# Performance work log

Hardware: AMD Instinct MI355X
Metric: run time of the kernel (lower is better)

The kernel has to match this reference:

```python
import jax, jax.numpy as jnp
import numpy as np

TAU = 1.0  # forward() default temperature

def setup_inputs() -> dict:
    key = jax.random.key(0)
    ks = jax.random.split(key, 6)
    B, T, I, H, O = 1024, 512, 100, 150, 3
    s_ih = 1.0 / np.sqrt(H)  # torch nn.RNN init scale (uniform +-1/sqrt(H)); randn used for simplicity of magnitude
    return {
        "x": jax.random.normal(ks[0], (B, T, I), dtype=jnp.float32),
        "h0": jax.random.normal(ks[1], (B, H), dtype=jnp.float32),  # init=True: h ~ N(0,1)
        "g": jax.random.normal(ks[2], (B, T, O), dtype=jnp.float32),  # gumbel noise (externalized)
        "W_ih": jax.random.normal(ks[3], (H, I), dtype=jnp.float32) * s_ih,
        "W_hh": jax.random.normal(ks[4], (H, H), dtype=jnp.float32) * s_ih,
        "W_fc": jax.random.normal(ks[5], (O, H), dtype=jnp.float32) * s_ih,
    }

def _rnn_relu(x, h0, W_ih, W_hh):
    # x: [B,T,I]; precompute input projection once (batched GEMM), then scan over time.
    xw = jnp.einsum("bti,hi->tbh", x, W_ih)  # [T,B,H]
    def step(h, xw_t):
        h = jax.nn.relu(xw_t + h @ W_hh.T)
        return h, h
    _, hs = jax.lax.scan(step, h0, xw)  # hs: [T,B,H]
    return jnp.transpose(hs, (1, 0, 2))  # [B,T,H]

def reference(x, h0, g, W_ih, W_hh, W_fc):
    hidden = _rnn_relu(x, h0, W_ih, W_hh)           # [B,T,H]
    logits = jnp.einsum("bth,oh->bto", hidden, W_fc)  # [B,T,O]
    # F.gumbel_softmax(hard=True): softmax((logits+g)/tau), straight-through one-hot
    y_soft = jax.nn.softmax((logits + g) / TAU, axis=-1)
    idx = jnp.argmax(y_soft, axis=-1)
    y_hard = jax.nn.one_hot(idx, logits.shape[-1], dtype=y_soft.dtype)
    out = y_soft + jax.lax.stop_gradient(y_hard - y_soft)
    return (out, hidden, logits)
```

## Files before the change

kernel.cpp:

```cpp
#include <hip/hip_runtime.h>

constexpr int NB = 1024;
constexpr int NT = 512;
constexpr int NI = 100;
constexpr int NH = 150;
constexpr int NO = 3;
constexpr int KP = 256;
constexpr int XOFF = 152;
constexpr int ROWS = 2;
constexpr int KG   = 16;
constexpr int NCH  = 4;
constexpr int NJ   = 5;
constexpr int NTH  = 512;

template<int CTRL>
__device__ __forceinline__ float dpp_add(float v) {
    int t = __builtin_amdgcn_update_dpp(0, __float_as_int(v), CTRL, 0xF, 0xF, true);
    return v + __int_as_float(t);
}

__global__ __launch_bounds__(NTH, 2)
void rnn_fused(const float* __restrict__ x, const float* __restrict__ h0,
               const float* __restrict__ g, const float* __restrict__ Wih,
               const float* __restrict__ Whh, const float* __restrict__ Wfc,
               float* __restrict__ out, float* __restrict__ hidden,
               float* __restrict__ logits)
{
    __shared__ __align__(16) float hx[2][ROWS * KP];
    __shared__ float lg[2][ROWS][4];

    const int tid  = threadIdx.x;
    const int lane = tid & 63;
    const int wv   = tid >> 6;
    const int kg   = lane & 15;
    const int oq   = lane >> 4;
    const int oi   = wv * 4 + oq;
    const int row0 = blockIdx.x * ROWS;

    float Wreg[NJ][NCH][4];
#pragma unroll
    for (int j = 0; j < NJ; ++j) {
        const int o = oi + 32 * j;
#pragma unroll
        for (int i = 0; i < NCH; ++i) {
#pragma unroll
            for (int q = 0; q < 4; ++q) {
                const int k = 4 * (kg + KG * i) + q;
                float v = 0.f;
                if (o < NH) {
                    if (k < NH) v = Whh[o * NH + k];
                    else if (k >= XOFF && k < XOFF + NI) v = Wih[o * NI + (k - XOFF)];
                } else if (o < NH + NO) {
                    if (k < NH) v = Wfc[(o - NH) * NH + k];
                }
                Wreg[j][i][q] = v;
            }
        }
    }

    for (int e = tid; e < ROWS * NH; e += NTH) {
        int b = e / NH, k = e - b * NH;
        hx[0][b * KP + k] = h0[(row0 + b) * NH + k];
    }
    for (int e = tid; e < ROWS * NI; e += NTH) {
        int b = e / NI, i = e - b * NI;
        hx[0][b * KP + XOFF + i] = x[((size_t)(row0 + b) * NT + 0) * NI + i];
    }
    if (tid < 2 * ROWS * 6) {
        int u = tid; int f = u / (ROWS * 6); u -= f * (ROWS * 6);
        int b = u / 6, z = u - b * 6;
        int k = (z < 2) ? (NH + z) : (252 + z - 2);
        hx[f][b * KP + k] = 0.f;
    }
    __syncthreads();

    const int xb = (tid / 25) & 1, xq = tid - (tid / 25) * 25;
    const float* xrow = x + ((size_t)(row0 + xb) * NT) * NI + 4 * xq;
    float* hidb = hidden + ((size_t)(row0 + (kg & 1)) * NT) * NH;
    const float* grow = g + ((size_t)(row0 + (tid & 1)) * NT) * NO;
    const size_t emitb = ((size_t)(row0 + (tid & 1)) * NT) * NO;

    auto stepf = [&](int t, const float* __restrict__ cur, float* __restrict__ nxt,
                     float (*__restrict__ lgb)[4]) {
        float4 xp = make_float4(0.f, 0.f, 0.f, 0.f);
        const bool do_x = (tid < 50) && (t < NT - 1);
        if (do_x) xp = *reinterpret_cast<const float4*>(xrow + (size_t)(t + 1) * NI);
        float g0 = 0.f, g1 = 0.f, g2 = 0.f;
        const bool do_e = (tid < ROWS) && (t >= 1);
        if (do_e) {
            const float* gp = grow + (size_t)(t - 1) * NO;
            g0 = gp[0]; g1 = gp[1]; g2 = gp[2];
        }

        const float4* cur4 = reinterpret_cast<const float4*>(cur) + kg;
        float acc[NJ][ROWS];
#pragma unroll
        for (int j = 0; j < NJ; ++j)
#pragma unroll
            for (int b = 0; b < ROWS; ++b) acc[j][b] = 0.f;

#pragma unroll
        for (int i = 0; i < NCH; ++i) {
#pragma unroll
            for (int b = 0; b < ROWS; ++b) {
                const float4 hv = cur4[b * (KP / 4) + KG * i];
#pragma unroll
                for (int j = 0; j < NJ; ++j) {
                    acc[j][b] += Wreg[j][i][0] * hv.x;
                    acc[j][b] += Wreg[j][i][1] * hv.y;
                    acc[j][b] += Wreg[j][i][2] * hv.z;
                    acc[j][b] += Wreg[j][i][3] * hv.w;
                }
            }
        }

#pragma unroll
        for (int j = 0; j < NJ; ++j)
#pragma unroll
            for (int b = 0; b < ROWS; ++b) {
                float v = acc[j][b];
                v = dpp_add<0xB1>(v);
                v = dpp_add<0x4E>(v);
                v = dpp_add<0x141>(v);
                v = dpp_add<0x140>(v);
                acc[j][b] = v;
            }

        if (kg < ROWS) {
            const int b = kg;
#pragma unroll
            for (int j = 0; j < NJ; ++j) {
                const int o = oi + 32 * j;
                if (o < NH) {
                    if (t < NT) {
                        float v = fmaxf(acc[j][b], 0.f);
                        nxt[b * KP + o] = v;
                        hidb[(size_t)t * NH + o] = v;
                    }
                } else if (o < NH + NO) {
                    lgb[b][o - NH] = acc[j][b];
                }
            }
        }
        if (do_x) *reinterpret_cast<float4*>(nxt + xb * KP + XOFF + 4 * xq) = xp;
        __syncthreads();

        if (do_e) {
            float l0 = lgb[tid][0], l1 = lgb[tid][1], l2 = lgb[tid][2];
            float s0 = l0 + g0, s1 = l1 + g1, s2 = l2 + g2;
            int am = 0; float best = s0;
            if (s1 > best) { best = s1; am = 1; }
            if (s2 > best) { am = 2; }
            size_t base = emitb + (size_t)(t - 1) * NO;
            out[base + 0] = (am == 0) ? 1.f : 0.f;
            out[base + 1] = (am == 1) ? 1.f : 0.f;
            out[base + 2] = (am == 2) ? 1.f : 0.f;
            logits[base + 0] = l0;
            logits[base + 1] = l1;
            logits[base + 2] = l2;
        }
    };

    for (int t = 0; t < NT; t += 2) {
        stepf(t,     hx[0], hx[1], lg[0]);
        stepf(t + 1, hx[1], hx[0], lg[1]);
    }
    stepf(NT, hx[0], hx[1], lg[0]);
}

extern "C" void kernel_launch(void* const* d_in, const int* in_sizes, int n_in,
                              void* d_out, int out_size, void* d_ws, size_t ws_size,
                              hipStream_t stream) {
    const float* x   = (const float*)d_in[0];
    const float* h0  = (const float*)d_in[1];
    const float* g   = (const float*)d_in[2];
    const float* Wih = (const float*)d_in[3];
    const float* Whh = (const float*)d_in[4];
    const float* Wfc = (const float*)d_in[5];

    float* out    = (float*)d_out;
    float* hidden = out + (size_t)NB * NT * NO;
    float* logits = hidden + (size_t)NB * NT * NH;

    hipLaunchKernelGGL(rnn_fused, dim3(NB / ROWS), dim3(NTH), 0, stream,
                       x, h0, g, Wih, Whh, Wfc, out, hidden, logits);
}
```

Before: 1.829 ms.

## Split input projection into separate GEMM kernel and shrink recurrent matvec

Adds a GEMM kernel that computes x·W_ih^T for all timesteps up front into a workspace buffer. The recurrent kernel then handles only the 150-wide hidden state, with 4 batch rows per block and 8-lane reductions instead of 16. The old fused kernel stays as a fallback when no workspace is available. This shortens the serial critical path per step, at the cost of roughly 300MB of extra global traffic to write and read the projection buffer.

```diff
diff --git a/kernel.cpp b/kernel.cpp
--- a/kernel.cpp
+++ b/kernel.cpp
@@ -5,13 +5,6 @@
 constexpr int NI = 100;
 constexpr int NH = 150;
 constexpr int NO = 3;
-constexpr int KP = 256;
-constexpr int XOFF = 152;
-constexpr int ROWS = 2;
-constexpr int KG   = 16;
-constexpr int NCH  = 4;
-constexpr int NJ   = 5;
-constexpr int NTH  = 512;
 
 template<int CTRL>
 __device__ __forceinline__ float dpp_add(float v) {
@@ -19,6 +12,204 @@
     return v + __int_as_float(t);
 }
 
+constexpr int GB = 128, GH = 32, GT = 256;
+__global__ __launch_bounds__(GT, 2)
+void xw_gemm(const float* __restrict__ x, const float* __restrict__ Wih,
+             float* __restrict__ xw)
+{
+    __shared__ __align__(16) float xt[GB * NI];
+    __shared__ __align__(16) float ot[GB * GH];
+    const int tid = threadIdx.x;
+    const int b0 = blockIdx.x * GB, t = blockIdx.y, h0 = blockIdx.z * GH;
+
+    for (int e = tid; e < GB * (NI / 4); e += GT) {
+        int r = e / 25, c = e - r * 25;
+        reinterpret_cast<float4*>(xt)[r * 25 + c] =
+            reinterpret_cast<const float4*>(x + ((size_t)(b0 + r) * NT + t) * NI)[c];
+    }
+    __syncthreads();
+
+    const int row = tid & (GB - 1);
+    const int hbase = __builtin_amdgcn_readfirstlane(h0 + (tid >> 7) * 16);
+    const float* wrow[16];
+#pragma unroll
+    for (int j = 0; j < 16; ++j) {
+        int h = hbase + j;
+        wrow[j] = Wih + (size_t)(h < NH ? h : NH - 1) * NI;
+    }
+    float acc[16];
+#pragma unroll
+    for (int j = 0; j < 16; ++j) acc[j] = 0.f;
+
+    const float4* xr = reinterpret_cast<const float4*>(xt) + row * 25;
+#pragma unroll 5
+    for (int k4 = 0; k4 < 25; ++k4) {
+        const float4 xv = xr[k4];
+#pragma unroll
+        for (int j = 0; j < 16; ++j) {
+            const float4 wv = reinterpret_cast<const float4*>(wrow[j])[k4];
+            acc[j] += wv.x * xv.x;
+            acc[j] += wv.y * xv.y;
+            acc[j] += wv.z * xv.z;
+            acc[j] += wv.w * xv.w;
+        }
+    }
+    const int hg = (tid >> 7) * 16;
+#pragma unroll
+    for (int j = 0; j < 16; ++j) ot[row * GH + hg + j] = acc[j];
+    __syncthreads();
+
+    for (int e = tid; e < GB * 16; e += GT) {
+        int r = e >> 4, p = e & 15, h = h0 + 2 * p;
+        if (h < NH) {
+            float2 v = *reinterpret_cast<const float2*>(&ot[r * GH + 2 * p]);
+            *reinterpret_cast<float2*>(&xw[((size_t)t * NB + b0 + r) * NH + h]) = v;
+        }
+    }
+}
+
+constexpr int KP2 = 160, ROWS2 = 4, NTH2 = 512;
+__global__ __launch_bounds__(NTH2, 2)
+void rnn_rec(const float* __restrict__ xw, const float* __restrict__ h0v,
+             const float* __restrict__ g, const float* __restrict__ Whh,
+             const float* __restrict__ Wfc, float* __restrict__ out,
+             float* __restrict__ hidden, float* __restrict__ logits)
+{
+    __shared__ __align__(16) float hx[2][ROWS2 * KP2];
+    __shared__ float lg[2][ROWS2][4];
+
+    const int tid = threadIdx.x, lane = tid & 63, wv = tid >> 6;
+    const int kg = lane & 7, oq = lane >> 3, oi = wv * 8 + oq;
+    const int row0 = blockIdx.x * ROWS2;
+
+    float Wreg[3][5][4];
+#pragma unroll
+    for (int j = 0; j < 3; ++j) {
+        const int o = oi + 64 * j;
+#pragma unroll
+        for (int i = 0; i < 5; ++i)
+#pragma unroll
+            for (int q = 0; q < 4; ++q) {
+                const int k = 4 * (kg + 8 * i) + q;
+                float v = 0.f;
+                if (k < NH) {
+                    if (o < NH) v = Whh[o * NH + k];
+                    else if (o < NH + NO) v = Wfc[(o - NH) * NH + k];
+                }
+                Wreg[j][i][q] = v;
+            }
+    }
+
+    for (int e = tid; e < ROWS2 * NH; e += NTH2) {
+        int b = e / NH, k = e - b * NH;
+        hx[0][b * KP2 + k] = h0v[(row0 + b) * NH + k];
+    }
+    if (tid < 2 * ROWS2 * 10) {
+        int u = tid, f = u / (ROWS2 * 10); u -= f * (ROWS2 * 10);
+        int b = u / 10, z = u - b * 10;
+        hx[f][b * KP2 + NH + z] = 0.f;
+    }
+    __syncthreads();
+
+    const float* xwb = xw + (size_t)(row0 + (kg & 3)) * NH;
+    float* hidb = hidden + (size_t)(row0 + (kg & 3)) * NT * NH;
+    const float* grow = g + (size_t)(row0 + (tid & 3)) * NT * NO;
+    const size_t emitb = (size_t)(row0 + (tid & 3)) * NT * NO;
+
+    auto stepf = [&](int t, const float* __restrict__ cur, float* __restrict__ nxt,
+                     float (*__restrict__ lgb)[4]) {
+        float xwv[3] = {0.f, 0.f, 0.f};
+        const bool wr = (kg < ROWS2);
+        if (wr && t < NT) {
+            const float* xp = xwb + (size_t)t * (NB * NH);
+#pragma unroll
+            for (int j = 0; j < 3; ++j) {
+                const int o = oi + 64 * j;
+                if (o < NH) xwv[j] = xp[o];
+            }
+        }
+        float g0 = 0.f, g1 = 0.f, g2 = 0.f;
+        const bool de = (tid < ROWS2) && (t >= 1);
+        if (de) {
+            const float* gp = grow + (size_t)(t - 1) * NO;
+            g0 = gp[0]; g1 = gp[1]; g2 = gp[2];
+        }
+
+        const float4* cur4 = reinterpret_cast<const float4*>(cur) + kg;
+        float acc[3][ROWS2];
+#pragma unroll
+        for (int j = 0; j < 3; ++j)
+#pragma unroll
+            for (int b = 0; b < ROWS2; ++b) acc[j][b] = 0.f;
+
+#pragma unroll
+        for (int i = 0; i < 5; ++i)
+#pragma unroll
+            for (int b = 0; b < ROWS2; ++b) {
+                const float4 hv = cur4[b * (KP2 / 4) + 8 * i];
+#pragma unroll
+                for (int j = 0; j < 3; ++j) {
+                    acc[j][b] += Wreg[j][i][0] * hv.x;
+                    acc[j][b] += Wreg[j][i][1] * hv.y;
+                    acc[j][b] += Wreg[j][i][2] * hv.z;
+                    acc[j][b] += Wreg[j][i][3] * hv.w;
+                }
+            }
+
+#pragma unroll
+        for (int j = 0; j < 3; ++j)
+#pragma unroll
+            for (int b = 0; b < ROWS2; ++b) {
+                float v = acc[j][b];
+                v = dpp_add<0xB1>(v);
+                v = dpp_add<0x4E>(v);
+                v = dpp_add<0x141>(v);
+                acc[j][b] = v;
+            }
+
+        if (wr) {
+            const int b = kg;
+#pragma unroll
+            for (int j = 0; j < 3; ++j) {
+                const int o = oi + 64 * j;
+                if (o < NH) {
+                    if (t < NT) {
+                        float v = fmaxf(acc[j][b] + xwv[j], 0.f);
+                        nxt[b * KP2 + o] = v;
+                        hidb[(size_t)t * NH + o] = v;
+                    }
+                } else if (o < NH + NO) {
+                    lgb[b][o - NH] = acc[j][b];
+                }
+            }
+        }
+        __syncthreads();
+
+        if (de) {
+            float l0 = lgb[tid][0], l1 = lgb[tid][1], l2 = lgb[tid][2];
+            float s0 = l0 + g0, s1 = l1 + g1, s2 = l2 + g2;
+            int am = 0; float best = s0;
+            if (s1 > best) { best = s1; am = 1; }
+            if (s2 > best) { am = 2; }
+            size_t base = emitb + (size_t)(t - 1) * NO;
+            out[base + 0] = (am == 0) ? 1.f : 0.f;
+            out[base + 1] = (am == 1) ? 1.f : 0.f;
+            out[base + 2] = (am == 2) ? 1.f : 0.f;
+            logits[base + 0] = l0;
+            logits[base + 1] = l1;
+            logits[base + 2] = l2;
+        }
+    };
+
+    for (int t = 0; t < NT; t += 2) {
+        stepf(t,     hx[0], hx[1], lg[0]);
+        stepf(t + 1, hx[1], hx[0], lg[1]);
+    }
+    stepf(NT, hx[0], hx[1], lg[0]);
+}
+
+namespace fb {
+constexpr int KP = 256, XOFF = 152, ROWS = 2, KG = 16, NCH = 4, NJ = 5, NTH = 512;
 __global__ __launch_bounds__(NTH, 2)
 void rnn_fused(const float* __restrict__ x, const float* __restrict__ h0,
                const float* __restrict__ g, const float* __restrict__ Wih,
@@ -28,21 +219,15 @@
 {
     __shared__ __align__(16) float hx[2][ROWS * KP];
     __shared__ float lg[2][ROWS][4];
-
-    const int tid  = threadIdx.x;
-    const int lane = tid & 63;
-    const int wv   = tid >> 6;
-    const int kg   = lane & 15;
-    const int oq   = lane >> 4;
-    const int oi   = wv * 4 + oq;
+    const int tid = threadIdx.x, lane = tid & 63, wv = tid >> 6;
+    const int kg = lane & 15, oq = lane >> 4, oi = wv * 4 + oq;
     const int row0 = blockIdx.x * ROWS;
-
     float Wreg[NJ][NCH][4];
 #pragma unroll
     for (int j = 0; j < NJ; ++j) {
         const int o = oi + 32 * j;
 #pragma unroll
-        for (int i = 0; i < NCH; ++i) {
+        for (int i = 0; i < NCH; ++i)
 #pragma unroll
             for (int q = 0; q < 4; ++q) {
                 const int k = 4 * (kg + KG * i) + q;
@@ -55,9 +240,7 @@
                 }
                 Wreg[j][i][q] = v;
             }
-        }
-    }
-
+    }
     for (int e = tid; e < ROWS * NH; e += NTH) {
         int b = e / NH, k = e - b * NH;
         hx[0][b * KP + k] = h0[(row0 + b) * NH + k];
@@ -73,13 +256,11 @@
         hx[f][b * KP + k] = 0.f;
     }
     __syncthreads();
-
     const int xb = (tid / 25) & 1, xq = tid - (tid / 25) * 25;
     const float* xrow = x + ((size_t)(row0 + xb) * NT) * NI + 4 * xq;
     float* hidb = hidden + ((size_t)(row0 + (kg & 1)) * NT) * NH;
     const float* grow = g + ((size_t)(row0 + (tid & 1)) * NT) * NO;
     const size_t emitb = ((size_t)(row0 + (tid & 1)) * NT) * NO;
-
     auto stepf = [&](int t, const float* __restrict__ cur, float* __restrict__ nxt,
                      float (*__restrict__ lgb)[4]) {
         float4 xp = make_float4(0.f, 0.f, 0.f, 0.f);
@@ -91,16 +272,14 @@
             const float* gp = grow + (size_t)(t - 1) * NO;
             g0 = gp[0]; g1 = gp[1]; g2 = gp[2];
         }
-
         const float4* cur4 = reinterpret_cast<const float4*>(cur) + kg;
         float acc[NJ][ROWS];
 #pragma unroll
         for (int j = 0; j < NJ; ++j)
 #pragma unroll
             for (int b = 0; b < ROWS; ++b) acc[j][b] = 0.f;
-
-#pragma unroll
-        for (int i = 0; i < NCH; ++i) {
+#pragma unroll
+        for (int i = 0; i < NCH; ++i)
 #pragma unroll
             for (int b = 0; b < ROWS; ++b) {
                 const float4 hv = cur4[b * (KP / 4) + KG * i];
@@ -112,8 +291,6 @@
                     acc[j][b] += Wreg[j][i][3] * hv.w;
                 }
             }
-        }
-
 #pragma unroll
         for (int j = 0; j < NJ; ++j)
 #pragma unroll
@@ -125,7 +302,6 @@
                 v = dpp_add<0x140>(v);
                 acc[j][b] = v;
             }
-
         if (kg < ROWS) {
             const int b = kg;
 #pragma unroll
@@ -144,7 +320,6 @@
         }
         if (do_x) *reinterpret_cast<float4*>(nxt + xb * KP + XOFF + 4 * xq) = xp;
         __syncthreads();
-
         if (do_e) {
             float l0 = lgb[tid][0], l1 = lgb[tid][1], l2 = lgb[tid][2];
             float s0 = l0 + g0, s1 = l1 + g1, s2 = l2 + g2;
@@ -160,12 +335,12 @@
             logits[base + 2] = l2;
         }
     };
-
     for (int t = 0; t < NT; t += 2) {
         stepf(t,     hx[0], hx[1], lg[0]);
         stepf(t + 1, hx[1], hx[0], lg[1]);
     }
     stepf(NT, hx[0], hx[1], lg[0]);
+}
 }
 
 extern "C" void kernel_launch(void* const* d_in, const int* in_sizes, int n_in,
@@ -182,6 +357,15 @@
     float* hidden = out + (size_t)NB * NT * NO;
     float* logits = hidden + (size_t)NB * NT * NH;
 
-    hipLaunchKernelGGL(rnn_fused, dim3(NB / ROWS), dim3(NTH), 0, stream,
-                       x, h0, g, Wih, Whh, Wfc, out, hidden, logits);
-}
+    const size_t need = (size_t)NT * NB * NH * sizeof(float);
+    if (d_ws != nullptr && ws_size >= need) {
+        float* xwbuf = (float*)d_ws;
+        hipLaunchKernelGGL(xw_gemm, dim3(NB / GB, NT, (NH + GH - 1) / GH), dim3(GT),
+                           0, stream, x, Wih, xwbuf);
+        hipLaunchKernelGGL(rnn_rec, dim3(NB / ROWS2), dim3(NTH2), 0, stream,
+                           xwbuf, h0, g, Whh, Wfc, out, hidden, logits);
+    } else {
+        hipLaunchKernelGGL(fb::rnn_fused, dim3(NB / fb::ROWS), dim3(fb::NTH), 0, stream,
+                           x, h0, g, Wih, Whh, Wfc, out, hidden, logits);
+    }
+}
```

Measured after the change: 2.213 ms. +21.0%, slower.

## Split input projection into separate GEMM kernel and prefetch xw asynchronously

Applied to the files above, without the earlier changes.

Moves the x·W_ih projection out of the sequential recurrence into a parallel GEMM kernel that writes a [T,B,H] buffer in the workspace. The recurrent kernel then handles one batch row per 256-thread block, multiplies only W_hh (K=150 instead of 250), and prefetches the next timestep's projected input into LDS with global_load_lds. This shortens the serial critical path per step and raises block count. The cost is an extra ~300MB workspace round trip to global memory. The old fused kernel stays as a fallback when the workspace is too small.

```diff
diff --git a/kernel.cpp b/kernel.cpp
--- a/kernel.cpp
+++ b/kernel.cpp
@@ -5,13 +5,6 @@
 constexpr int NI = 100;
 constexpr int NH = 150;
 constexpr int NO = 3;
-constexpr int KP = 256;
-constexpr int XOFF = 152;
-constexpr int ROWS = 2;
-constexpr int KG   = 16;
-constexpr int NCH  = 4;
-constexpr int NJ   = 5;
-constexpr int NTH  = 512;
 
 template<int CTRL>
 __device__ __forceinline__ float dpp_add(float v) {
@@ -19,6 +12,182 @@
     return v + __int_as_float(t);
 }
 
+__device__ __forceinline__ void async_copy_f32(const float* src, float* lds_dst) {
+    __builtin_amdgcn_global_load_lds(
+        (const __attribute__((address_space(1))) void*)src,
+        (__attribute__((address_space(3))) void*)lds_dst, 4, 0, 0);
+}
+
+constexpr int XR = 64, XTH = 512;
+__global__ __launch_bounds__(XTH, 1)
+void xw_gemm(const float* __restrict__ x, const float* __restrict__ Wih,
+             float* __restrict__ xw)
+{
+    __shared__ __align__(16) float Wl[152 * NI];
+    __shared__ float xT[XR * 101];
+    __shared__ float ot[XR * 151];
+    const int tid = threadIdx.x;
+    const int b0 = blockIdx.x * XR;
+    const int t  = blockIdx.y;
+
+    for (int e = tid; e < 152 * 25; e += XTH) {
+        int wr = e / 25, k4 = e - wr * 25;
+        float4 v = make_float4(0.f, 0.f, 0.f, 0.f);
+        if (wr < NH) v = *reinterpret_cast<const float4*>(Wih + (size_t)wr * NI + 4 * k4);
+        *reinterpret_cast<float4*>(&Wl[wr * NI + 4 * k4]) = v;
+    }
+    for (int e = tid; e < XR * 25; e += XTH) {
+        int r = e / 25, k4 = e - r * 25;
+        float4 v = *reinterpret_cast<const float4*>(x + ((size_t)(b0 + r) * NT + t) * NI + 4 * k4);
+        xT[r * 101 + 4 * k4 + 0] = v.x; xT[r * 101 + 4 * k4 + 1] = v.y;
+        xT[r * 101 + 4 * k4 + 2] = v.z; xT[r * 101 + 4 * k4 + 3] = v.w;
+    }
+    __syncthreads();
+
+    const int row = tid & 63;
+    const int wv  = tid >> 6;
+    float acc[19];
+#pragma unroll
+    for (int j = 0; j < 19; ++j) acc[j] = 0.f;
+    const float* xr = &xT[row * 101];
+    const float* wb = &Wl[19 * wv * NI];
+    for (int k4 = 0; k4 < 25; ++k4) {
+        const float x0 = xr[4 * k4 + 0], x1 = xr[4 * k4 + 1];
+        const float x2 = xr[4 * k4 + 2], x3 = xr[4 * k4 + 3];
+#pragma unroll
+        for (int j = 0; j < 19; ++j) {
+            const float4 w4 = *reinterpret_cast<const float4*>(&wb[j * NI + 4 * k4]);
+            acc[j] += w4.x * x0; acc[j] += w4.y * x1;
+            acc[j] += w4.z * x2; acc[j] += w4.w * x3;
+        }
+    }
+#pragma unroll
+    for (int j = 0; j < 19; ++j) {
+        const int h = 19 * wv + j;
+        if (h < NH) ot[row * 151 + h] = acc[j];
+    }
+    __syncthreads();
+
+    for (int e = tid; e < XR * 75; e += XTH) {
+        int r = e / 75, c2 = e - r * 75;
+        float2 v = make_float2(ot[r * 151 + 2 * c2], ot[r * 151 + 2 * c2 + 1]);
+        *reinterpret_cast<float2*>(&xw[((size_t)t * NB + b0 + r) * NH + 2 * c2]) = v;
+    }
+}
+
+constexpr int RTH = 256;
+__global__ __launch_bounds__(RTH, 4)
+void rnn_rec(const float* __restrict__ xw, const float* __restrict__ h0v,
+             const float* __restrict__ g, const float* __restrict__ Whh,
+             const float* __restrict__ Wfc, float* __restrict__ out,
+             float* __restrict__ hidden, float* __restrict__ logits)
+{
+    __shared__ __align__(16) float hx[2][160];
+    __shared__ __align__(16) float xq[2][152];
+    __shared__ float lg[2][4];
+
+    const int tid = threadIdx.x, lane = tid & 63, wv = tid >> 6;
+    const int kg = lane & 7, oq = lane >> 3;
+    const int oi = wv * 8 + oq;
+    const int row = blockIdx.x;
+
+    float Wreg[5][5][4];
+#pragma unroll
+    for (int j = 0; j < 5; ++j) {
+        const int o = oi + 32 * j;
+#pragma unroll
+        for (int i = 0; i < 5; ++i)
+#pragma unroll
+            for (int q = 0; q < 4; ++q) {
+                const int k = 4 * (kg + 8 * i) + q;
+                float v = 0.f;
+                if (k < NH) {
+                    if (o < NH) v = Whh[o * NH + k];
+                    else if (o < NH + NO) v = Wfc[(o - NH) * NH + k];
+                }
+                Wreg[j][i][q] = v;
+            }
+    }
+
+    if (tid < NH) hx[0][tid] = h0v[(size_t)row * NH + tid];
+    if (tid < 20) { int f = tid / 10, z = tid - 10 * (tid / 10); hx[f][NH + z] = 0.f; }
+    {
+        const float* s = xw + (size_t)row * NH;
+        if (tid < 64) { async_copy_f32(s + tid, &xq[0][0]); async_copy_f32(s + 64 + tid, &xq[0][64]); }
+        if (tid < 22) async_copy_f32(s + 128 + tid, &xq[0][128]);
+    }
+    __syncthreads();
+
+    float* hidb = hidden + (size_t)row * NT * NH;
+    const float* gb = g + (size_t)row * NT * NO;
+    float* ob = out + (size_t)row * NT * NO;
+    float* lb = logits + (size_t)row * NT * NO;
+
+    auto stepf = [&](int t, const float* __restrict__ cur, float* __restrict__ nxt,
+                     float* __restrict__ lgc, const float* __restrict__ xv,
+                     float* __restrict__ xnxt) {
+        if (t + 1 < NT) {
+            const float* s = xw + ((size_t)(t + 1) * NB + row) * NH;
+            if (tid < 64) { async_copy_f32(s + tid, xnxt); async_copy_f32(s + 64 + tid, xnxt + 64); }
+            if (tid < 22) async_copy_f32(s + 128 + tid, xnxt + 128);
+        }
+        float acc[5];
+#pragma unroll
+        for (int j = 0; j < 5; ++j) acc[j] = 0.f;
+        const float4* c4 = reinterpret_cast<const float4*>(cur);
+#pragma unroll
+        for (int i = 0; i < 5; ++i) {
+            const float4 hv = c4[kg + 8 * i];
+#pragma unroll
+            for (int j = 0; j < 5; ++j) {
+                acc[j] += Wreg[j][i][0] * hv.x; acc[j] += Wreg[j][i][1] * hv.y;
+                acc[j] += Wreg[j][i][2] * hv.z; acc[j] += Wreg[j][i][3] * hv.w;
+            }
+        }
+#pragma unroll
+        for (int j = 0; j < 5; ++j) {
+            float v = acc[j];
+            v = dpp_add<0xB1>(v); v = dpp_add<0x4E>(v); v = dpp_add<0x141>(v);
+            acc[j] = v;
+        }
+        if (kg == 0) {
+#pragma unroll
+            for (int j = 0; j < 5; ++j) {
+                const int o = oi + 32 * j;
+                if (o < NH) {
+                    if (t < NT) {
+                        float v = fmaxf(acc[j] + xv[o], 0.f);
+                        nxt[o] = v;
+                        hidb[(size_t)t * NH + o] = v;
+                    }
+                } else if (o < NH + NO) lgc[o - NH] = acc[j];
+            }
+        }
+        __syncthreads();
+        if (tid == 0 && t >= 1) {
+            float l0 = lgc[0], l1 = lgc[1], l2 = lgc[2];
+            const float* gp = gb + (size_t)(t - 1) * NO;
+            float s0 = l0 + gp[0], s1 = l1 + gp[1], s2 = l2 + gp[2];
+            int am = 0; float best = s0;
+            if (s1 > best) { best = s1; am = 1; }
+            if (s2 > best) am = 2;
+            size_t base = (size_t)(t - 1) * NO;
+            ob[base + 0] = (am == 0) ? 1.f : 0.f;
+            ob[base + 1] = (am == 1) ? 1.f : 0.f;
+            ob[base + 2] = (am == 2) ? 1.f : 0.f;
+            lb[base + 0] = l0; lb[base + 1] = l1; lb[base + 2] = l2;
+        }
+    };
+
+    for (int t = 0; t < NT; t += 2) {
+        stepf(t,     hx[0], hx[1], lg[0], xq[0], xq[1]);
+        stepf(t + 1, hx[1], hx[0], lg[1], xq[1], xq[0]);
+    }
+    stepf(NT, hx[0], hx[1], lg[0], xq[0], xq[1]);
+}
+
+namespace fb {
+constexpr int KP = 256, XOFF = 152, ROWS = 2, KG = 16, NCH = 4, NJ = 5, NTH = 512;
 __global__ __launch_bounds__(NTH, 2)
 void rnn_fused(const float* __restrict__ x, const float* __restrict__ h0,
                const float* __restrict__ g, const float* __restrict__ Wih,
@@ -28,21 +197,15 @@
 {
     __shared__ __align__(16) float hx[2][ROWS * KP];
     __shared__ float lg[2][ROWS][4];
-
-    const int tid  = threadIdx.x;
-    const int lane = tid & 63;
-    const int wv   = tid >> 6;
-    const int kg   = lane & 15;
-    const int oq   = lane >> 4;
-    const int oi   = wv * 4 + oq;
+    const int tid = threadIdx.x, lane = tid & 63, wv = tid >> 6;
+    const int kg = lane & 15, oq = lane >> 4, oi = wv * 4 + oq;
     const int row0 = blockIdx.x * ROWS;
-
     float Wreg[NJ][NCH][4];
 #pragma unroll
     for (int j = 0; j < NJ; ++j) {
         const int o = oi + 32 * j;
 #pragma unroll
-        for (int i = 0; i < NCH; ++i) {
+        for (int i = 0; i < NCH; ++i)
 #pragma unroll
             for (int q = 0; q < 4; ++q) {
                 const int k = 4 * (kg + KG * i) + q;
@@ -55,9 +218,7 @@
                 }
                 Wreg[j][i][q] = v;
             }
-        }
-    }
-
+    }
     for (int e = tid; e < ROWS * NH; e += NTH) {
         int b = e / NH, k = e - b * NH;
         hx[0][b * KP + k] = h0[(row0 + b) * NH + k];
@@ -73,13 +234,11 @@
         hx[f][b * KP + k] = 0.f;
     }
     __syncthreads();
-
     const int xb = (tid / 25) & 1, xq = tid - (tid / 25) * 25;
     const float* xrow = x + ((size_t)(row0 + xb) * NT) * NI + 4 * xq;
     float* hidb = hidden + ((size_t)(row0 + (kg & 1)) * NT) * NH;
     const float* grow = g + ((size_t)(row0 + (tid & 1)) * NT) * NO;
     const size_t emitb = ((size_t)(row0 + (tid & 1)) * NT) * NO;
-
     auto stepf = [&](int t, const float* __restrict__ cur, float* __restrict__ nxt,
                      float (*__restrict__ lgb)[4]) {
         float4 xp = make_float4(0.f, 0.f, 0.f, 0.f);
@@ -91,16 +250,14 @@
             const float* gp = grow + (size_t)(t - 1) * NO;
             g0 = gp[0]; g1 = gp[1]; g2 = gp[2];
         }
-
         const float4* cur4 = reinterpret_cast<const float4*>(cur) + kg;
         float acc[NJ][ROWS];
 #pragma unroll
         for (int j = 0; j < NJ; ++j)
 #pragma unroll
             for (int b = 0; b < ROWS; ++b) acc[j][b] = 0.f;
-
-#pragma unroll
-        for (int i = 0; i < NCH; ++i) {
+#pragma unroll
+        for (int i = 0; i < NCH; ++i)
 #pragma unroll
             for (int b = 0; b < ROWS; ++b) {
                 const float4 hv = cur4[b * (KP / 4) + KG * i];
@@ -112,20 +269,15 @@
                     acc[j][b] += Wreg[j][i][3] * hv.w;
                 }
             }
-        }
-
 #pragma unroll
         for (int j = 0; j < NJ; ++j)
 #pragma unroll
             for (int b = 0; b < ROWS; ++b) {
                 float v = acc[j][b];
-                v = dpp_add<0xB1>(v);
-                v = dpp_add<0x4E>(v);
-                v = dpp_add<0x141>(v);
-                v = dpp_add<0x140>(v);
+                v = dpp_add<0xB1>(v); v = dpp_add<0x4E>(v);
+                v = dpp_add<0x141>(v); v = dpp_add<0x140>(v);
                 acc[j][b] = v;
             }
-
         if (kg < ROWS) {
             const int b = kg;
 #pragma unroll
@@ -144,7 +296,6 @@
         }
         if (do_x) *reinterpret_cast<float4*>(nxt + xb * KP + XOFF + 4 * xq) = xp;
         __syncthreads();
-
         if (do_e) {
             float l0 = lgb[tid][0], l1 = lgb[tid][1], l2 = lgb[tid][2];
             float s0 = l0 + g0, s1 = l1 + g1, s2 = l2 + g2;
@@ -160,12 +311,12 @@
             logits[base + 2] = l2;
         }
     };
-
     for (int t = 0; t < NT; t += 2) {
         stepf(t,     hx[0], hx[1], lg[0]);
         stepf(t + 1, hx[1], hx[0], lg[1]);
     }
     stepf(NT, hx[0], hx[1], lg[0]);
+}
 }
 
 extern "C" void kernel_launch(void* const* d_in, const int* in_sizes, int n_in,
@@ -182,6 +333,15 @@
     float* hidden = out + (size_t)NB * NT * NO;
     float* logits = hidden + (size_t)NB * NT * NH;
 
-    hipLaunchKernelGGL(rnn_fused, dim3(NB / ROWS), dim3(NTH), 0, stream,
-                       x, h0, g, Wih, Whh, Wfc, out, hidden, logits);
-}
+    const size_t need = (size_t)NT * NB * NH * sizeof(float);
+    if (d_ws != nullptr && ws_size >= need) {
+        float* xwbuf = (float*)d_ws;
+        hipLaunchKernelGGL(xw_gemm, dim3(NB / XR, NT), dim3(XTH), 0, stream,
+                           x, Wih, xwbuf);
+        hipLaunchKernelGGL(rnn_rec, dim3(NB), dim3(RTH), 0, stream,
+                           xwbuf, h0, g, Whh, Wfc, out, hidden, logits);
+    } else {
+        hipLaunchKernelGGL(fb::rnn_fused, dim3(NB / fb::ROWS), dim3(fb::NTH), 0, stream,
+                           x, h0, g, Wih, Whh, Wfc, out, hidden, logits);
+    }
+}
```

Measured after the change: 1.558 ms. -14.8%, faster.
